# Kernel tuning notes

Hardware: AMD Instinct MI355X
Metric: run time of the kernel (lower is better)

Reference implementation:

```python
import jax, jax.numpy as jnp
import numpy as np

NX, NZ = 256, 256   # grid size
NT = 400            # time steps
NS = 4              # shots (batched wavefields)
NR = 128            # receivers
DX = DZ = 10.0      # grid spacing (m)
DT = 1.0e-3         # time step (s)
F0 = 10.0           # dominant frequency (Hz)
NABC = 30           # absorbing boundary width (cells)


def setup_inputs() -> dict:
    key = jax.random.key(0)
    k1, k2, k3, k4 = jax.random.split(key, 4)
    # velocity 1500-4000 m/s, density 1000-2000 kg/m^3
    vp = 1500.0 + 2500.0 * jax.random.uniform(k1, (NX, NZ), dtype=jnp.float32)
    rho = 1000.0 + 1000.0 * jax.random.uniform(k2, (NX, NZ), dtype=jnp.float32)
    # PML-style quadratic damping profile (bc_pml analogue)
    ix = np.arange(NX, dtype=np.float64)
    iz = np.arange(NZ, dtype=np.float64)
    dist_x = np.maximum(np.maximum(NABC - ix, ix - (NX - 1 - NABC)), 0.0) / NABC
    dist_z = np.maximum(np.maximum(NABC - iz, iz - (NZ - 1 - NABC)), 0.0) / NABC
    d0 = 3.0 * 4000.0 * np.log(1000.0) / (2.0 * NABC * DX)
    damp = jnp.asarray(d0 * (dist_x[:, None] ** 2 + dist_z[None, :] ** 2), dtype=jnp.float32)
    # Ricker wavelet, one trace per shot
    t = np.arange(NT) * DT - 1.2 / F0
    a = (np.pi * F0 * t) ** 2
    wav = ((1.0 - 2.0 * a) * np.exp(-a)).astype(np.float32)
    wavelet = jnp.tile(jnp.asarray(wav)[None, :], (NS, 1))
    src_x = jax.random.randint(k3, (NS,), NABC + 2, NX - NABC - 2)
    src_z = jnp.full((NS,), NABC + 2, dtype=jnp.int32)
    rcv_x = jnp.sort(jax.random.randint(k4, (NR,), NABC + 2, NX - NABC - 2))
    rcv_z = jnp.full((NR,), NABC + 2, dtype=jnp.int32)
    return dict(vp=vp, rho=rho, damp=damp, wavelet=wavelet,
                src_x=src_x, src_z=src_z, rcv_x=rcv_x, rcv_z=rcv_z)


# staggered-grid first-order differences (zero-padded at boundary)
def _dxf(a):
    return jnp.pad(a[:, 1:, :] - a[:, :-1, :], ((0, 0), (0, 1), (0, 0)))

def _dxb(a):
    return jnp.pad(a[:, 1:, :] - a[:, :-1, :], ((0, 0), (1, 0), (0, 0)))

def _dzf(a):
    return jnp.pad(a[:, :, 1:] - a[:, :, :-1], ((0, 0), (0, 0), (0, 1)))

def _dzb(a):
    return jnp.pad(a[:, :, 1:] - a[:, :, :-1], ((0, 0), (0, 0), (1, 0)))


def reference(vp, rho, damp, wavelet, src_x, src_z, rcv_x, rcv_z):
    """Stress-velocity acoustic FD propagator with absorbing damping.
    Returns recorded pressure at receivers: [src_n, nt, rcv_n]."""
    ns = wavelet.shape[0]
    nx, nz = vp.shape
    kappa = rho * vp * vp          # bulk modulus [nx, nz]
    fac = 1.0 - DT * damp          # damping factor [nx, nz]
    binv = DT / rho                # buoyancy * dt
    shot = jnp.arange(ns)
    src_amp = DT / (DX * DZ)

    def step(carry, wav_t):
        p, vx, vz = carry
        vx = fac * vx - binv * _dxf(p) / DX
        vz = fac * vz - binv * _dzf(p) / DZ
        p = fac * p - DT * kappa * (_dxb(vx) / DX + _dzb(vz) / DZ)
        p = p.at[shot, src_x, src_z].add(wav_t * src_amp)
        rec = p[:, rcv_x, rcv_z]   # [ns, nr]
        return (p, vx, vz), rec

    zero = jnp.zeros((ns, nx, nz), vp.dtype)
    _, recs = jax.lax.scan(step, (zero, zero, zero), wavelet.T)  # [nt, ns, nr]
    return jnp.transpose(recs, (1, 0, 2))
```

## Files before the change

kernel.cpp:

```cpp
#include <hip/hip_runtime.h>


#define NXc 256
#define NZc 256
#define NTc 400
#define NSc 4
#define NRc 128

#define TS 8
#define Bt 32
#define NSTR 12
#define BT 576
#define LROW 48
#define LSZ ((48 + 2) * LROW)
#define NBLK (NSc * 64)
#define NEP (NTc / TS)

constexpr float DT_H    = 0.001f;
constexpr float INV_D   = 0.1f;
constexpr float SRC_AMP = 0.001f * 0.01f;
constexpr int   NXZ     = NXc * NZc;

typedef float f32x4 __attribute__((ext_vector_type(4)));

__global__ __launch_bounds__(BT) void prop_kernel(
    float* __restrict__ xchg, unsigned* __restrict__ flags,
    const float* __restrict__ vp, const float* __restrict__ rho,
    const float* __restrict__ damp, const float* __restrict__ wavelet,
    const int* __restrict__ src_x, const int* __restrict__ src_z,
    const int* __restrict__ rcv_x, const int* __restrict__ rcv_z,
    float* __restrict__ out)
{
    __shared__ float sp[LSZ], svx[LSZ];
    __shared__ float spE[BT + 1], svzE[BT + 1];

    const int tid  = threadIdx.x;
    const int bid  = blockIdx.x;
    const int s    = bid >> 6;
    const int tile = bid & 63;
    const int tx = tile >> 3, tz = tile & 7;
    const int gx0 = tx * Bt - TS, gz0 = tz * Bt - TS;

    const int li  = tid / NSTR;
    const int st  = tid - li * NSTR;
    const int lk0 = st * 4;
    const int gi  = gx0 + li;
    const int gk0 = gz0 + lk0;
    const bool in = ((unsigned)gi < (unsigned)NXc) &&
                    ((unsigned)gk0 < (unsigned)NZc);
    const int c4 = s * NXZ + gi * NZc + gk0;
    const bool central = in && ((unsigned)(li - TS) < (unsigned)Bt)
                            && (lk0 >= TS) && (lk0 <= TS + Bt - 4);
    const bool ring = in && !central;

    const size_t F = (size_t)NSc * NXZ;
    float* b0 = xchg;
    float* b1 = xchg + 3 * F;

    float pr[4]  = {0, 0, 0, 0};
    float vxr[4] = {0, 0, 0, 0};
    float vzr[4] = {0, 0, 0, 0};
    float fr[4], bxr[4], bzr[4], dkxr[4], dkzr[4], sfr[4];
    {
        const int sx = src_x[s], sz = src_z[s];
        if (in) {
            float4 r4 = *(const float4*)(rho  + c4 - s * NXZ);
            float4 v4 = *(const float4*)(vp   + c4 - s * NXZ);
            float4 d4 = *(const float4*)(damp + c4 - s * NXZ);
            float rv[4] = {r4.x, r4.y, r4.z, r4.w};
            float vv[4] = {v4.x, v4.y, v4.z, v4.w};
            float dv[4] = {d4.x, d4.y, d4.z, d4.w};
#pragma unroll
            for (int k = 0; k < 4; ++k) {
                int gk = gk0 + k;
                fr[k] = 1.0f - DT_H * dv[k];
                float bi = DT_H / rv[k] * INV_D;
                bxr[k] = (gi == NXc - 1) ? 0.f : bi;
                bzr[k] = (gk == NZc - 1) ? 0.f : bi;
                float dk = DT_H * rv[k] * vv[k] * vv[k] * INV_D;
                dkxr[k] = (gi == 0) ? 0.f : dk;
                dkzr[k] = (gk == 0) ? 0.f : dk;
                sfr[k]  = (gi == sx && gk == sz) ? SRC_AMP : 0.f;
            }
        } else {
#pragma unroll
            for (int k = 0; k < 4; ++k) {
                fr[k] = 0.f; bxr[k] = 0.f; bzr[k] = 0.f;
                dkxr[k] = 0.f; dkzr[k] = 0.f; sfr[k] = 0.f;
            }
        }
    }

    if (tid < LROW) {
        sp[tid] = 0.f; svx[tid] = 0.f;
        sp[LSZ - LROW + tid] = 0.f; svx[LSZ - LROW + tid] = 0.f;
    }
    if (tid == 0) { svzE[0] = 0.f; spE[BT] = 0.f; }

    int rxv = 0, rzv = 0;
    if (tid < NRc) { rxv = rcv_x[tid]; rzv = rcv_z[tid]; }
    const bool rown = (tid < NRc) &&
        ((unsigned)(rxv - tx * Bt) < (unsigned)Bt) &&
        ((unsigned)(rzv - tz * Bt) < (unsigned)Bt);
    const int rj = (rxv - gx0 + 1) * LROW + (rzv - gz0);
    float* obase = out + (size_t)s * NTc * NRc + tid;
    const float* wb = wavelet + s * NTc;

    int nbid = -1;
    if (tid < 9) {
        int dx = tid / 3 - 1, dz = tid - (tid / 3) * 3 - 1;
        if (dx != 0 || dz != 0) {
            int nx2 = tx + dx, nz2 = tz + dz;
            if (((unsigned)nx2 < 8u) && ((unsigned)nz2 < 8u))
                nbid = (s << 6) + nx2 * 8 + nz2;
        }
    }

    const int jb = (li + 1) * LROW + lk0;

    for (int l = 0; l < NEP; ++l) {
        *(float4*)&sp[jb] = make_float4(pr[0], pr[1], pr[2], pr[3]);
        spE[tid] = pr[0];
        __syncthreads();

        for (int tau = 0; tau < TS; ++tau) {
            float4 pn4 = *(const float4*)&sp[jb + LROW];
            float  pze = spE[tid + 1];
            float pnx[4] = {pn4.x, pn4.y, pn4.z, pn4.w};
            float pz1[4] = {pr[1], pr[2], pr[3], pze};
#pragma unroll
            for (int k = 0; k < 4; ++k) {
                vxr[k] = fr[k] * vxr[k] - bxr[k] * (pnx[k] - pr[k]);
                vzr[k] = fr[k] * vzr[k] - bzr[k] * (pz1[k] - pr[k]);
            }
            *(float4*)&svx[jb] = make_float4(vxr[0], vxr[1], vxr[2], vxr[3]);
            svzE[tid + 1] = vzr[3];
            __syncthreads();

            const float wv = wb[l * TS + tau];
            float4 vxm4 = *(const float4*)&svx[jb - LROW];
            float  vzm0 = svzE[tid];
            float vxm[4] = {vxm4.x, vxm4.y, vxm4.z, vxm4.w};
            float vzm[4] = {vzm0, vzr[0], vzr[1], vzr[2]};
#pragma unroll
            for (int k = 0; k < 4; ++k) {
                pr[k] = fr[k] * pr[k]
                      - dkxr[k] * (vxr[k] - vxm[k])
                      - dkzr[k] * (vzr[k] - vzm[k])
                      + sfr[k] * wv;
            }
            *(float4*)&sp[jb] = make_float4(pr[0], pr[1], pr[2], pr[3]);
            spE[tid] = pr[0];
            __syncthreads();

            if (rown) obase[(size_t)(l * TS + tau) * NRc] = sp[rj];
        }

        if (l < NEP - 1) {
            float* pb = (l & 1) ? b1 : b0;
            if (central) {
                f32x4 a = {pr[0], pr[1], pr[2], pr[3]};
                f32x4 b = {vxr[0], vxr[1], vxr[2], vxr[3]};
                f32x4 c = {vzr[0], vzr[1], vzr[2], vzr[3]};
                asm volatile(
                    "global_store_dwordx4 %0, %3, off sc0 sc1\n\t"
                    "global_store_dwordx4 %1, %4, off sc0 sc1\n\t"
                    "global_store_dwordx4 %2, %5, off sc0 sc1"
                    :: "v"(pb + c4), "v"(pb + F + c4), "v"(pb + 2 * F + c4),
                       "v"(a), "v"(b), "v"(c)
                    : "memory");
            }
            asm volatile("s_waitcnt vmcnt(0)" ::: "memory");
            __syncthreads();
            if (tid == 0) {
                unsigned val = (unsigned)(l + 1);
                asm volatile("global_store_dword %0, %1, off sc0 sc1"
                             :: "v"(flags + bid), "v"(val) : "memory");
            }
            if (nbid >= 0) {
                const unsigned* fp = flags + nbid;
                const unsigned want = (unsigned)(l + 1);
                while (true) {
                    unsigned v;
                    asm volatile("global_load_dword %0, %1, off sc0 sc1\n\t"
                                 "s_waitcnt vmcnt(0)"
                                 : "=&v"(v) : "v"(fp) : "memory");
                    if (v >= want) break;
                    __builtin_amdgcn_s_sleep(1);
                }
            }
            __syncthreads();
            if (ring) {
                f32x4 a, b, c;
                asm volatile(
                    "global_load_dwordx4 %0, %3, off sc0 sc1\n\t"
                    "global_load_dwordx4 %1, %4, off sc0 sc1\n\t"
                    "global_load_dwordx4 %2, %5, off sc0 sc1\n\t"
                    "s_waitcnt vmcnt(0)"
                    : "=&v"(a), "=&v"(b), "=&v"(c)
                    : "v"(pb + c4), "v"(pb + F + c4), "v"(pb + 2 * F + c4)
                    : "memory");
                pr[0] = a.x; pr[1] = a.y; pr[2] = a.z; pr[3] = a.w;
                vxr[0] = b.x; vxr[1] = b.y; vxr[2] = b.z; vxr[3] = b.w;
                vzr[0] = c.x; vzr[1] = c.y; vzr[2] = c.z; vzr[3] = c.w;
            }
        }
    }
}

extern "C" void kernel_launch(void* const* d_in, const int* in_sizes, int n_in,
                              void* d_out, int out_size, void* d_ws, size_t ws_size,
                              hipStream_t stream)
{
    const float* vp      = (const float*)d_in[0];
    const float* rho     = (const float*)d_in[1];
    const float* damp    = (const float*)d_in[2];
    const float* wavelet = (const float*)d_in[3];
    const int*   src_x   = (const int*)d_in[4];
    const int*   src_z   = (const int*)d_in[5];
    const int*   rcv_x   = (const int*)d_in[6];
    const int*   rcv_z   = (const int*)d_in[7];
    float* out = (float*)d_out;
    float* ws  = (float*)d_ws;

    const size_t F = (size_t)NSc * NXZ;
    float* xchg = ws;
    unsigned* flags = (unsigned*)(ws + 6 * F);

    hipMemsetAsync(flags, 0, NBLK * sizeof(unsigned), stream);

    prop_kernel<<<NBLK, BT, 0, stream>>>(
        xchg, flags, vp, rho, damp, wavelet,
        src_x, src_z, rcv_x, rcv_z, out);
}
```

Measured before the change: 343.3 us.

## Let each halo thread poll only its owning neighbor flag and issue exchange stores earlier

Ring (halo) threads now each spin on the flag of the specific neighbor tile that owns their cells, and then load immediately. The previous scheme had up to eight threads poll neighbor flags and then hit a block-wide barrier before any halo load. The global exchange stores move into the last inner time step, before its shared-memory barrier, so their latency overlaps that barrier. The receiver write for the last step is deferred past the flag store. This removes one block barrier per epoch, but many threads now poll flags concurrently, which adds memory traffic.

```diff
diff --git a/kernel.cpp b/kernel.cpp
--- a/kernel.cpp
+++ b/kernel.cpp
@@ -22,6 +22,17 @@
 constexpr int   NXZ     = NXc * NZc;
 
 typedef float f32x4 __attribute__((ext_vector_type(4)));
+
+__device__ __forceinline__ unsigned ldu_far(const unsigned* p) {
+    unsigned v;
+    asm volatile("global_load_dword %0, %1, off sc0 sc1\n\t"
+                 "s_waitcnt vmcnt(0)" : "=&v"(v) : "v"(p) : "memory");
+    return v;
+}
+__device__ __forceinline__ void stu_far(unsigned* p, unsigned v) {
+    asm volatile("global_store_dword %0, %1, off sc0 sc1"
+                 :: "v"(p), "v"(v) : "memory");
+}
 
 __global__ __launch_bounds__(BT) void prop_kernel(
     float* __restrict__ xchg, unsigned* __restrict__ flags,
@@ -106,19 +117,16 @@
     float* obase = out + (size_t)s * NTc * NRc + tid;
     const float* wb = wavelet + s * NTc;
 
-    int nbid = -1;
-    if (tid < 9) {
-        int dx = tid / 3 - 1, dz = tid - (tid / 3) * 3 - 1;
-        if (dx != 0 || dz != 0) {
-            int nx2 = tx + dx, nz2 = tz + dz;
-            if (((unsigned)nx2 < 8u) && ((unsigned)nz2 < 8u))
-                nbid = (s << 6) + nx2 * 8 + nz2;
-        }
-    }
+    const int sdx = (li  < TS) ? -1 : (li  < TS + Bt) ? 0 : 1;
+    const int sdz = (lk0 < TS) ? -1 : (lk0 < TS + Bt) ? 0 : 1;
+    const int snb = (s << 6) + (tx + sdx) * 8 + (tz + sdz);
 
     const int jb = (li + 1) * LROW + lk0;
 
     for (int l = 0; l < NEP; ++l) {
+        const bool notLast = (l < NEP - 1);
+        float* pb = (l & 1) ? b1 : b0;
+
         *(float4*)&sp[jb] = make_float4(pr[0], pr[1], pr[2], pr[3]);
         spE[tid] = pr[0];
         __syncthreads();
@@ -149,16 +157,7 @@
                       - dkzr[k] * (vzr[k] - vzm[k])
                       + sfr[k] * wv;
             }
-            *(float4*)&sp[jb] = make_float4(pr[0], pr[1], pr[2], pr[3]);
-            spE[tid] = pr[0];
-            __syncthreads();
-
-            if (rown) obase[(size_t)(l * TS + tau) * NRc] = sp[rj];
-        }
-
-        if (l < NEP - 1) {
-            float* pb = (l & 1) ? b1 : b0;
-            if (central) {
+            if (tau == TS - 1 && notLast && central) {
                 f32x4 a = {pr[0], pr[1], pr[2], pr[3]};
                 f32x4 b = {vxr[0], vxr[1], vxr[2], vxr[3]};
                 f32x4 c = {vzr[0], vzr[1], vzr[2], vzr[3]};
@@ -170,27 +169,23 @@
                        "v"(a), "v"(b), "v"(c)
                     : "memory");
             }
+            *(float4*)&sp[jb] = make_float4(pr[0], pr[1], pr[2], pr[3]);
+            spE[tid] = pr[0];
+            __syncthreads();
+
+            if (tau < TS - 1 && rown)
+                obase[(size_t)(l * TS + tau) * NRc] = sp[rj];
+        }
+
+        if (notLast) {
             asm volatile("s_waitcnt vmcnt(0)" ::: "memory");
             __syncthreads();
-            if (tid == 0) {
-                unsigned val = (unsigned)(l + 1);
-                asm volatile("global_store_dword %0, %1, off sc0 sc1"
-                             :: "v"(flags + bid), "v"(val) : "memory");
-            }
-            if (nbid >= 0) {
-                const unsigned* fp = flags + nbid;
+            if (tid == 0) stu_far(flags + bid, (unsigned)(l + 1));
+            if (rown) obase[(size_t)(l * TS + TS - 1) * NRc] = sp[rj];
+            if (ring) {
                 const unsigned want = (unsigned)(l + 1);
-                while (true) {
-                    unsigned v;
-                    asm volatile("global_load_dword %0, %1, off sc0 sc1\n\t"
-                                 "s_waitcnt vmcnt(0)"
-                                 : "=&v"(v) : "v"(fp) : "memory");
-                    if (v >= want) break;
-                    __builtin_amdgcn_s_sleep(1);
-                }
-            }
-            __syncthreads();
-            if (ring) {
+                const unsigned* fp = flags + snb;
+                while (ldu_far(fp) < want) __builtin_amdgcn_s_sleep(1);
                 f32x4 a, b, c;
                 asm volatile(
                     "global_load_dwordx4 %0, %3, off sc0 sc1\n\t"
@@ -200,10 +195,12 @@
                     : "=&v"(a), "=&v"(b), "=&v"(c)
                     : "v"(pb + c4), "v"(pb + F + c4), "v"(pb + 2 * F + c4)
                     : "memory");
-                pr[0] = a.x; pr[1] = a.y; pr[2] = a.z; pr[3] = a.w;
-                vxr[0] = b.x; vxr[1] = b.y; vxr[2] = b.z; vxr[3] = b.w;
-                vzr[0] = c.x; vzr[1] = c.y; vzr[2] = c.z; vzr[3] = c.w;
-            }
+                pr[0]=a.x; pr[1]=a.y; pr[2]=a.z; pr[3]=a.w;
+                vxr[0]=b.x; vxr[1]=b.y; vxr[2]=b.z; vxr[3]=b.w;
+                vzr[0]=c.x; vzr[1]=c.y; vzr[2]=c.z; vzr[3]=c.w;
+            }
+        } else {
+            if (rown) obase[(size_t)(l * TS + TS - 1) * NRc] = sp[rj];
         }
     }
 }
```

New measurement: 368.0 us. 1.07x slower.
